# Kernel optimization log

Measured on AMD Instinct MI355X. Metric: run time of the kernel, lower is better.

## Reference

```python
import jax, jax.numpy as jnp
import numpy as np

N, INT_DIM = 4096, 512
X_DIMS = [128, 128, 128, 128]
DIM_LIST = list(zip(X_DIMS[:-1], X_DIMS[1:]))
TOT_DIM = sum(d0 * d1 + d1 for d0, d1 in DIM_LIST)  # 49536
FUNS = [jax.nn.relu, jax.nn.relu, None]


def setup_inputs() -> dict:
    key = jax.random.key(0)
    k1, k2, k3, k4 = jax.random.split(key, 4)
    int_x = jax.random.normal(k1, (N, INT_DIM), dtype=jnp.float32)
    x = jax.random.normal(k2, (N, X_DIMS[0]), dtype=jnp.float32)
    # torch Linear(IntDim, tot_dim): W [out, in], b [out]; scale like kaiming-uniform-ish
    W = jax.random.normal(k3, (TOT_DIM, INT_DIM), dtype=jnp.float32) * (1.0 / np.sqrt(INT_DIM))
    b = jax.random.normal(k4, (TOT_DIM,), dtype=jnp.float32) * 0.02
    return {"int_x": int_x, "x": x, "W": W, "b": b}


def reference(int_x, x, W, b):
    # hypernetwork: per-sample generated weights/biases, [N, tot_dim]
    temp = jnp.einsum('ni,oi->no', int_x, W) + b
    cum = 0
    h = x
    for (d0, d1), fun in zip(DIM_LIST, FUNS):
        bias = temp[:, cum:cum + d1]                                   # [N, d1]
        weight = temp[:, cum + d1:cum + d1 + d0 * d1].reshape(-1, d0, d1)  # [N, d0, d1]
        cum += d1 + d0 * d1
        h = jnp.einsum('npq,np->nq', weight, h) + bias
        if fun is not None:
            h = fun(h)
    return h
```

## Files before the change

kernel.cpp:

```cpp
#include <hip/hip_runtime.h>
#include <cstdint>
#include <cstddef>

#define NSAMP 4096
#define KDIM  512
#define TOT   49536
#define NUMN  387
#define BK    64

typedef __attribute__((ext_vector_type(8))) __bf16 bf16x8;
typedef __attribute__((ext_vector_type(4))) __bf16 bf16x4;
typedef __attribute__((ext_vector_type(4))) float  f32x4;

#define AS1 __attribute__((address_space(1)))
#define AS3 __attribute__((address_space(3)))

__global__ void cast_bf16(const float* __restrict__ in, __bf16* __restrict__ out, int n4) {
    int i = blockIdx.x * blockDim.x + threadIdx.x;
    int stride = gridDim.x * blockDim.x;
    for (; i < n4; i += stride) {
        float4 v = ((const float4*)in)[i];
        bf16x4 o = { (__bf16)v.x, (__bf16)v.y, (__bf16)v.z, (__bf16)v.w };
        ((bf16x4*)out)[i] = o;
    }
}

__global__ __launch_bounds__(256) void hyper_gemm(
    const __bf16* __restrict__ A, const __bf16* __restrict__ B,
    const float* __restrict__ bias, __bf16* __restrict__ C)
{
    __shared__ __bf16 As[128 * BK];
    __shared__ __bf16 Bs[128 * BK];

    const int tid   = threadIdx.x;
    const int lane  = tid & 63;
    const int quad  = lane >> 4;
    const int r16   = lane & 15;
    const int wv    = tid >> 6;
    const int waveM = wv >> 1;
    const int waveN = wv & 1;

    const int num_m = gridDim.y;
    const int id    = blockIdx.y * NUMN + blockIdx.x;
    const int gsz   = 8 * num_m;
    const int s     = id / gsz;
    const int r     = id % gsz;
    const int base  = s * 8;
    int w = NUMN - base; if (w > 8) w = 8;
    const int n_t = base + r % w;
    const int m_t = r / w;

    const int m0 = m_t * 128;
    const int n0 = n_t * 128;

    f32x4 acc[4][4] = {};

    const __bf16* gAp[4];
    const __bf16* gBp[4];
    int ldsOff[4];
#pragma unroll
    for (int c = 0; c < 4; ++c) {
        int idx  = c * 256 + tid;
        int row  = idx >> 3;
        int gsrc = (idx & 7) ^ (row & 7);
        gAp[c] = A + (size_t)(m0 + row) * KDIM + gsrc * 8;
        gBp[c] = B + (size_t)(n0 + row) * KDIM + gsrc * 8;
        ldsOff[c] = idx * 8;
    }

    const int rsw = r16 & 7;

    for (int kt = 0; kt < KDIM / BK; ++kt) {
        const int k0 = kt * BK;
#pragma unroll
        for (int c = 0; c < 4; ++c) {
            __builtin_amdgcn_global_load_lds((AS1 void*)(gAp[c] + k0),
                (AS3 void*)(As + ldsOff[c]), 16, 0, 0);
            __builtin_amdgcn_global_load_lds((AS1 void*)(gBp[c] + k0),
                (AS3 void*)(Bs + ldsOff[c]), 16, 0, 0);
        }
        __syncthreads();

#pragma unroll
        for (int kk = 0; kk < 2; ++kk) {
            bf16x8 af[4], bf[4];
#pragma unroll
            for (int i = 0; i < 4; ++i) {
                int rr = waveM * 64 + i * 16 + r16;
                af[i] = *(const bf16x8*)(As + rr * BK + (((kk * 4 + quad) ^ rsw) * 8));
            }
#pragma unroll
            for (int j = 0; j < 4; ++j) {
                int rr = waveN * 64 + j * 16 + r16;
                bf[j] = *(const bf16x8*)(Bs + rr * BK + (((kk * 4 + quad) ^ rsw) * 8));
            }
#pragma unroll
            for (int i = 0; i < 4; ++i)
#pragma unroll
                for (int j = 0; j < 4; ++j)
                    acc[i][j] = __builtin_amdgcn_mfma_f32_16x16x32_bf16(af[i], bf[j], acc[i][j], 0, 0, 0);
        }
        __syncthreads();
    }

#pragma unroll
    for (int j = 0; j < 4; ++j) {
        int n = n0 + waveN * 64 + j * 16 + r16;
        float bb = bias[n];
#pragma unroll
        for (int i = 0; i < 4; ++i) {
            int mbase = m0 + waveM * 64 + i * 16 + quad * 4;
#pragma unroll
            for (int rr = 0; rr < 4; ++rr) {
                C[(size_t)(mbase + rr) * TOT + n] = (__bf16)(acc[i][j][rr] + bb);
            }
        }
    }
}

__global__ __launch_bounds__(256) void mlp_kernel(
    const float* __restrict__ x, const __bf16* __restrict__ temp,
    float* __restrict__ out, int samp0)
{
    const int n   = samp0 + blockIdx.x;
    const int tid = threadIdx.x;
    const int wv  = tid >> 6;
    const int l   = tid & 63;
    const int pg  = l >> 4;
    const int qg  = l & 15;

    __shared__ float h[128];
    __shared__ float partial[4][128];

    if (tid < 64) ((float2*)h)[tid] = ((const float2*)(x + (size_t)n * 128))[tid];

    const __bf16* row = temp + (size_t)blockIdx.x * TOT;
    int cum = 0;
#pragma unroll
    for (int layer = 0; layer < 3; ++layer) {
        const __bf16* bias = row + cum;
        const __bf16* wgt  = row + cum + 128;
        float acc[8] = {0, 0, 0, 0, 0, 0, 0, 0};
        __syncthreads();
#pragma unroll
        for (int i = 0; i < 8; ++i) {
            int p = wv * 32 + i * 4 + pg;
            bf16x8 w = *(const bf16x8*)(wgt + (size_t)p * 128 + qg * 8);
            float hp = h[p];
#pragma unroll
            for (int j = 0; j < 8; ++j) acc[j] += (float)w[j] * hp;
        }
#pragma unroll
        for (int j = 0; j < 8; ++j) {
            acc[j] += __shfl_xor(acc[j], 16);
            acc[j] += __shfl_xor(acc[j], 32);
        }
        if (pg == 0) {
#pragma unroll
            for (int j = 0; j < 8; ++j) partial[wv][qg * 8 + j] = acc[j];
        }
        __syncthreads();
        if (tid < 128) {
            float v = partial[0][tid] + partial[1][tid] + partial[2][tid] + partial[3][tid]
                    + (float)bias[tid];
            if (layer < 2) v = fmaxf(v, 0.f);
            h[tid] = v;
        }
        cum += 128 + 128 * 128;
    }
    __syncthreads();
    if (tid < 64) ((float2*)(out + (size_t)n * 128))[tid] = ((const float2*)h)[tid];
}

extern "C" void kernel_launch(void* const* d_in, const int* in_sizes, int n_in,
                              void* d_out, int out_size, void* d_ws, size_t ws_size,
                              hipStream_t stream) {
    const float* int_x = (const float*)d_in[0];
    const float* x     = (const float*)d_in[1];
    const float* W     = (const float*)d_in[2];
    const float* b     = (const float*)d_in[3];
    float* out = (float*)d_out;

    char* ws = (char*)d_ws;
    __bf16* A_bf = (__bf16*)ws;
    size_t offA = (size_t)NSAMP * KDIM * 2;
    __bf16* W_bf = (__bf16*)(ws + offA);
    size_t offW = offA + (size_t)TOT * KDIM * 2;
    __bf16* temp = (__bf16*)(ws + offW);

    size_t remain = (ws_size > offW) ? (ws_size - offW) : 0;
    int chunk = 128;
    for (int c = 1024; c >= 128; c >>= 1) {
        if ((size_t)c * TOT * 2 <= remain) { chunk = c; break; }
    }

    int nA4 = NSAMP * KDIM / 4;
    cast_bf16<<<(nA4 + 255) / 256, 256, 0, stream>>>(int_x, A_bf, nA4);
    int nW4 = TOT * KDIM / 4;
    cast_bf16<<<(nW4 + 255) / 256, 256, 0, stream>>>(W, W_bf, nW4);

    for (int samp0 = 0; samp0 < NSAMP; samp0 += chunk) {
        dim3 grid(NUMN, chunk / 128);
        hyper_gemm<<<grid, 256, 0, stream>>>(A_bf + (size_t)samp0 * KDIM, W_bf, b, temp);
        mlp_kernel<<<chunk, 256, 0, stream>>>(x, temp, out, samp0);
    }
}
```

Before: 541.6 us.

## Double-buffer LDS tiles in hyper_gemm to overlap global loads with MFMA

The shared-memory A and B tiles in the generator GEMM become two buffers. The next K-tile is issued with global_load_lds into the alternate buffer while MFMAs run on the current one, and one barrier per iteration replaces two. This aims to hide global-memory latency behind compute in the main GEMM. In exchange, LDS use per block doubles to 64 KB, which may lower occupancy.

```diff
diff --git a/kernel.cpp b/kernel.cpp
--- a/kernel.cpp
+++ b/kernel.cpp
@@ -29,8 +29,8 @@
     const __bf16* __restrict__ A, const __bf16* __restrict__ B,
     const float* __restrict__ bias, __bf16* __restrict__ C)
 {
-    __shared__ __bf16 As[128 * BK];
-    __shared__ __bf16 Bs[128 * BK];
+    __shared__ __bf16 As[2][128 * BK];
+    __shared__ __bf16 Bs[2][128 * BK];
 
     const int tid   = threadIdx.x;
     const int lane  = tid & 63;
@@ -70,16 +70,25 @@
 
     const int rsw = r16 & 7;
 
+#define STAGE(buf, kt)                                                        \
+    do {                                                                      \
+        const int _k0 = (kt) * BK;                                            \
+        _Pragma("unroll")                                                     \
+        for (int c = 0; c < 4; ++c) {                                         \
+            __builtin_amdgcn_global_load_lds((AS1 void*)(gAp[c] + _k0),       \
+                (AS3 void*)(&As[(buf)][ldsOff[c]]), 16, 0, 0);                \
+            __builtin_amdgcn_global_load_lds((AS1 void*)(gBp[c] + _k0),       \
+                (AS3 void*)(&Bs[(buf)][ldsOff[c]]), 16, 0, 0);                \
+        }                                                                     \
+    } while (0)
+
+    STAGE(0, 0);
+
+#pragma unroll 2
     for (int kt = 0; kt < KDIM / BK; ++kt) {
-        const int k0 = kt * BK;
-#pragma unroll
-        for (int c = 0; c < 4; ++c) {
-            __builtin_amdgcn_global_load_lds((AS1 void*)(gAp[c] + k0),
-                (AS3 void*)(As + ldsOff[c]), 16, 0, 0);
-            __builtin_amdgcn_global_load_lds((AS1 void*)(gBp[c] + k0),
-                (AS3 void*)(Bs + ldsOff[c]), 16, 0, 0);
-        }
+        const int cur = kt & 1;
         __syncthreads();
+        if (kt + 1 < KDIM / BK) STAGE(cur ^ 1, kt + 1);
 
 #pragma unroll
         for (int kk = 0; kk < 2; ++kk) {
@@ -87,12 +96,12 @@
 #pragma unroll
             for (int i = 0; i < 4; ++i) {
                 int rr = waveM * 64 + i * 16 + r16;
-                af[i] = *(const bf16x8*)(As + rr * BK + (((kk * 4 + quad) ^ rsw) * 8));
+                af[i] = *(const bf16x8*)(&As[cur][rr * BK + (((kk * 4 + quad) ^ rsw) * 8)]);
             }
 #pragma unroll
             for (int j = 0; j < 4; ++j) {
                 int rr = waveN * 64 + j * 16 + r16;
-                bf[j] = *(const bf16x8*)(Bs + rr * BK + (((kk * 4 + quad) ^ rsw) * 8));
+                bf[j] = *(const bf16x8*)(&Bs[cur][rr * BK + (((kk * 4 + quad) ^ rsw) * 8)]);
             }
 #pragma unroll
             for (int i = 0; i < 4; ++i)
@@ -100,8 +109,8 @@
                 for (int j = 0; j < 4; ++j)
                     acc[i][j] = __builtin_amdgcn_mfma_f32_16x16x32_bf16(af[i], bf[j], acc[i][j], 0, 0, 0);
         }
-        __syncthreads();
-    }
+    }
+#undef STAGE
 
 #pragma unroll
     for (int j = 0; j < 4; ++j) {
```

Measured after the change: 566.9 us. 1.05x slower.

## Load GEMM fragments directly from global into registers, dropping LDS staging

Applied to the files above, without the earlier changes.

The hypernetwork GEMM no longer stages A and B tiles through shared memory with global_load_lds and barriers. Each wave now loads its MFMA operand fragments straight from global memory into registers, fully unrolls the K loop, and software-prefetches the next k-slice. This removes the LDS traffic and the __syncthreads stalls. The cost is that the two waves sharing each A or B row block each fetch it from global/L2 separately, with 16-byte strided accesses per lane and higher register pressure.

```diff
diff --git a/kernel.cpp b/kernel.cpp
--- a/kernel.cpp
+++ b/kernel.cpp
@@ -6,14 +6,10 @@
 #define KDIM  512
 #define TOT   49536
 #define NUMN  387
-#define BK    64
 
 typedef __attribute__((ext_vector_type(8))) __bf16 bf16x8;
 typedef __attribute__((ext_vector_type(4))) __bf16 bf16x4;
 typedef __attribute__((ext_vector_type(4))) float  f32x4;
-
-#define AS1 __attribute__((address_space(1)))
-#define AS3 __attribute__((address_space(3)))
 
 __global__ void cast_bf16(const float* __restrict__ in, __bf16* __restrict__ out, int n4) {
     int i = blockIdx.x * blockDim.x + threadIdx.x;
@@ -29,9 +25,6 @@
     const __bf16* __restrict__ A, const __bf16* __restrict__ B,
     const float* __restrict__ bias, __bf16* __restrict__ C)
 {
-    __shared__ __bf16 As[128 * BK];
-    __shared__ __bf16 Bs[128 * BK];
-
     const int tid   = threadIdx.x;
     const int lane  = tid & 63;
     const int quad  = lane >> 4;
@@ -53,54 +46,44 @@
     const int m0 = m_t * 128;
     const int n0 = n_t * 128;
 
+    const __bf16* pA[4];
+    const __bf16* pB[4];
+#pragma unroll
+    for (int i = 0; i < 4; ++i)
+        pA[i] = A + (size_t)(m0 + waveM * 64 + i * 16 + r16) * KDIM + quad * 8;
+#pragma unroll
+    for (int j = 0; j < 4; ++j)
+        pB[j] = B + (size_t)(n0 + waveN * 64 + j * 16 + r16) * KDIM + quad * 8;
+
     f32x4 acc[4][4] = {};
 
-    const __bf16* gAp[4];
-    const __bf16* gBp[4];
-    int ldsOff[4];
+    bf16x8 a_cur[4], b_cur[4];
 #pragma unroll
-    for (int c = 0; c < 4; ++c) {
-        int idx  = c * 256 + tid;
-        int row  = idx >> 3;
-        int gsrc = (idx & 7) ^ (row & 7);
-        gAp[c] = A + (size_t)(m0 + row) * KDIM + gsrc * 8;
-        gBp[c] = B + (size_t)(n0 + row) * KDIM + gsrc * 8;
-        ldsOff[c] = idx * 8;
-    }
-
-    const int rsw = r16 & 7;
-
-    for (int kt = 0; kt < KDIM / BK; ++kt) {
-        const int k0 = kt * BK;
+    for (int i = 0; i < 4; ++i) a_cur[i] = *(const bf16x8*)(pA[i]);
 #pragma unroll
-        for (int c = 0; c < 4; ++c) {
-            __builtin_amdgcn_global_load_lds((AS1 void*)(gAp[c] + k0),
-                (AS3 void*)(As + ldsOff[c]), 16, 0, 0);
-            __builtin_amdgcn_global_load_lds((AS1 void*)(gBp[c] + k0),
-                (AS3 void*)(Bs + ldsOff[c]), 16, 0, 0);
-        }
-        __syncthreads();
+    for (int j = 0; j < 4; ++j) b_cur[j] = *(const bf16x8*)(pB[j]);
 
 #pragma unroll
-        for (int kk = 0; kk < 2; ++kk) {
-            bf16x8 af[4], bf[4];
+    for (int kt = 0; kt < KDIM / 32; ++kt) {
+        bf16x8 a_nxt[4], b_nxt[4];
+        if (kt + 1 < KDIM / 32) {
+            const int ko = (kt + 1) * 32;
 #pragma unroll
-            for (int i = 0; i < 4; ++i) {
-                int rr = waveM * 64 + i * 16 + r16;
-                af[i] = *(const bf16x8*)(As + rr * BK + (((kk * 4 + quad) ^ rsw) * 8));
-            }
+            for (int i = 0; i < 4; ++i) a_nxt[i] = *(const bf16x8*)(pA[i] + ko);
 #pragma unroll
-            for (int j = 0; j < 4; ++j) {
-                int rr = waveN * 64 + j * 16 + r16;
-                bf[j] = *(const bf16x8*)(Bs + rr * BK + (((kk * 4 + quad) ^ rsw) * 8));
-            }
+            for (int j = 0; j < 4; ++j) b_nxt[j] = *(const bf16x8*)(pB[j] + ko);
+        }
 #pragma unroll
-            for (int i = 0; i < 4; ++i)
+        for (int i = 0; i < 4; ++i)
 #pragma unroll
-                for (int j = 0; j < 4; ++j)
-                    acc[i][j] = __builtin_amdgcn_mfma_f32_16x16x32_bf16(af[i], bf[j], acc[i][j], 0, 0, 0);
+            for (int j = 0; j < 4; ++j)
+                acc[i][j] = __builtin_amdgcn_mfma_f32_16x16x32_bf16(a_cur[i], b_cur[j], acc[i][j], 0, 0, 0);
+        if (kt + 1 < KDIM / 32) {
+#pragma unroll
+            for (int i = 0; i < 4; ++i) a_cur[i] = a_nxt[i];
+#pragma unroll
+            for (int j = 0; j < 4; ++j) b_cur[j] = b_nxt[j];
         }
-        __syncthreads();
     }
 
 #pragma unroll
```

Result: slower. 1.004 ms (+85.3%).
